# Optimization experiments

Hardware: AMD Instinct MI355X
Metric: run time of the kernel (lower is better)

Reference implementation:

```python
import jax, jax.numpy as jnp
import numpy as np

TEMPLATE_SZ = 7
MAX_SR = 3


def setup_inputs() -> dict:
    key = jax.random.key(0)
    # image-like values in [0, 255) since the module ends with a uint8 cast
    x = jax.random.uniform(key, (2, 1, 192, 192), dtype=jnp.float32) * 255.0
    return {"inputs": x, "search_range": 3}


def reference(inputs, search_range):
    # Equivalent math to: pad(max_sr) -> unfold(k, pad=k//2) -> unfold(s) ->
    # permute -> slice sub-window -> reshape -> uint8.
    # Both zero-pads commute, so fold them into one pad and gather directly,
    # avoiding the huge duplicated double-im2col intermediate.
    k = TEMPLATE_SZ
    max_sr = MAX_SR
    cv = 2 * search_range + 1          # cost_volume_sz
    offset = max_sr - search_range
    B, C, H, W = inputs.shape          # C == 1 (implied by the torch view)
    pad = max_sr + k // 2              # combined zero padding
    Q = jnp.pad(inputs[:, 0].astype(jnp.float32), ((0, 0), (pad, pad), (pad, pad)))
    r = offset + jnp.arange(cv)        # search offsets within max window
    t = jnp.arange(k)                  # template offsets
    # windows[b,i,j,dy,dx,ty,tx] = Q[b, i + r[dy] + ty, j + r[dx] + tx]
    iy = jnp.arange(H)[:, None, None] + r[None, :, None] + t[None, None, :]  # [H, cv, k]
    jx = jnp.arange(W)[:, None, None] + r[None, :, None] + t[None, None, :]  # [W, cv, k]
    win = Q[:, iy[:, None, :, None, :, None], jx[None, :, None, :, None, :]]  # [B,H,W,cv,cv,k,k]
    return win.reshape(B, H, W, cv * cv, k * k).astype(jnp.uint8)
```

## Files before the change

### kernel.cpp

```cpp
#include <hip/hip_runtime.h>


#define KT 7
#define K2 49
#define MAX_SR 3
#define B_ 2
#define H_ 192
#define W_ 192
#define HW (H_ * W_)
#define PAD 6
#define NTHREADS 256
#define RMAX 10
#define PS 17
#define NBLOCKS 768
#define NGROUPS (B_ * H_ * W_ / 4)

typedef int vint4 __attribute__((ext_vector_type(4)));

__global__ __launch_bounds__(NTHREADS) void esw_kernel(
    const float* __restrict__ in, int* __restrict__ out,
    int cv, int offset, int d , int cvmagic )
{
    __shared__ int patch[13 * PS + 4];

    const int tid = threadIdx.x;
    const int bid = blockIdx.x;

    int fe[RMAX][4];
    #pragma unroll
    for (int r = 0; r < RMAX; ++r) {
        int j4 = 4 * (tid + NTHREADS * r);
        #pragma unroll
        for (int u = 0; u < 4; ++u) {
            int jj = j4 + u;
            if (jj >= 4 * d) jj = 4 * d - 1;
            int p_in = (jj >= d) + (jj >= 2 * d) + (jj >= 3 * d);
            int j  = jj - p_in * d;
            int rr = j / K2;
            int tt = j - rr * K2;
            int ry = (rr * cvmagic) >> 16;
            int rx = rr - ry * cv;
            int ty = tt / KT;
            int tx = tt - ty * KT;
            fe[r][u] = (offset + ry + ty) * PS + (offset + rx + tx) + p_in;
        }
    }

    for (int it = 0; it < NGROUPS / NBLOCKS; ++it) {
        const int g = it * NBLOCKS + bid;
        const int pix0 = 4 * g;
        const int b   = pix0 / HW;
        const int rem = pix0 - b * HW;
        const int h   = rem / W_;
        const int w   = rem - h * W_;

        __syncthreads();
        if (tid < 13 * 16) {
            int dy = tid >> 4;
            int dx = tid & 15;
            int y = h + dy - PAD;
            int x = w + dx - PAD;
            int v = 0;
            if ((unsigned)y < (unsigned)H_ && (unsigned)x < (unsigned)W_)
                v = (int)in[b * HW + y * W_ + x];
            patch[dy * PS + dx] = v;
        }
        __syncthreads();

        int* op = out + (long long)g * (long long)(4 * d);
        #pragma unroll
        for (int r = 0; r < RMAX; ++r) {
            int q = tid + NTHREADS * r;
            if (q < d) {
                vint4 v;
                v.x = patch[fe[r][0]];
                v.y = patch[fe[r][1]];
                v.z = patch[fe[r][2]];
                v.w = patch[fe[r][3]];
                *(vint4*)(op + 4 * q) = v;
            }
        }
    }
}

extern "C" void kernel_launch(void* const* d_in, const int* in_sizes, int n_in,
                              void* d_out, int out_size, void* d_ws, size_t ws_size,
                              hipStream_t stream) {
    const float* in = (const float*)d_in[0];
    int* out = (int*)d_out;

    int cv2 = out_size / (B_ * H_ * W_ * K2);
    int cv = 1;
    while (cv * cv < cv2) ++cv;
    int offset = MAX_SR - (cv - 1) / 2;
    int d = cv2 * K2;
    int cvmagic = 65536 / cv + 1;

    esw_kernel<<<NBLOCKS, NTHREADS, 0, stream>>>(in, out, cv, offset, d, cvmagic);
}
```

Before: 702.7 us.

## Precompute gather index table and launch one block per pixel group

Index offsets are computed once by a small separate kernel into workspace, and each esw block loads its offsets as vector loads instead of computing divisions per thread. The persistent loop over 768 blocks is replaced by one 512-thread block per 4-pixel group, which drops the per-iteration syncs and gives a much larger grid. Offsets are prescaled to bytes to save address arithmetic. In exchange it adds a second launch and a table read per block, and relies on workspace being available, falling back to inline computation otherwise.

```diff
diff --git a/kernel.cpp b/kernel.cpp
--- a/kernel.cpp
+++ b/kernel.cpp
@@ -9,76 +9,90 @@
 #define W_ 192
 #define HW (H_ * W_)
 #define PAD 6
-#define NTHREADS 256
-#define RMAX 10
+#define NT 512
+#define RMAX 5
 #define PS 17
-#define NBLOCKS 768
 #define NGROUPS (B_ * H_ * W_ / 4)
+#define TABN (4 * NT * RMAX)
 
 typedef int vint4 __attribute__((ext_vector_type(4)));
 
-__global__ __launch_bounds__(NTHREADS) void esw_kernel(
+__device__ __forceinline__ int tab_entry(int jj, int cv, int offset, int d,
+                                         int cvmagic) {
+    if (jj >= 4 * d) jj = 4 * d - 1;
+    int p_in = (jj >= d) + (jj >= 2 * d) + (jj >= 3 * d);
+    int j  = jj - p_in * d;
+    int rr = j / K2;
+    int tt = j - rr * K2;
+    int ry = (rr * cvmagic) >> 16;
+    int rx = rr - ry * cv;
+    int ty = tt / KT;
+    int tx = tt - ty * KT;
+    return 4 * ((offset + ry + ty) * PS + (offset + rx + tx) + p_in);
+}
+
+__global__ __launch_bounds__(256) void tab_kernel(
+    int* __restrict__ tab, int cv, int offset, int d, int cvmagic)
+{
+    int jj = blockIdx.x * 256 + threadIdx.x;
+    if (jj < TABN) tab[jj] = tab_entry(jj, cv, offset, d, cvmagic);
+}
+
+__global__ __launch_bounds__(NT, 6) void esw_kernel(
     const float* __restrict__ in, int* __restrict__ out,
-    int cv, int offset, int d , int cvmagic )
+    const int* __restrict__ tab,
+    int cv, int offset, int d, int cvmagic)
 {
     __shared__ int patch[13 * PS + 4];
 
     const int tid = threadIdx.x;
-    const int bid = blockIdx.x;
+    const int g   = blockIdx.x;
 
-    int fe[RMAX][4];
-    #pragma unroll
-    for (int r = 0; r < RMAX; ++r) {
-        int j4 = 4 * (tid + NTHREADS * r);
+    vint4 f[RMAX];
+    if (tab) {
         #pragma unroll
-        for (int u = 0; u < 4; ++u) {
-            int jj = j4 + u;
-            if (jj >= 4 * d) jj = 4 * d - 1;
-            int p_in = (jj >= d) + (jj >= 2 * d) + (jj >= 3 * d);
-            int j  = jj - p_in * d;
-            int rr = j / K2;
-            int tt = j - rr * K2;
-            int ry = (rr * cvmagic) >> 16;
-            int rx = rr - ry * cv;
-            int ty = tt / KT;
-            int tx = tt - ty * KT;
-            fe[r][u] = (offset + ry + ty) * PS + (offset + rx + tx) + p_in;
+        for (int r = 0; r < RMAX; ++r)
+            f[r] = *(const vint4*)(tab + 4 * (tid + NT * r));
+    } else {
+        #pragma unroll
+        for (int r = 0; r < RMAX; ++r) {
+            int j4 = 4 * (tid + NT * r);
+            #pragma unroll
+            for (int u = 0; u < 4; ++u)
+                f[r][u] = tab_entry(j4 + u, cv, offset, d, cvmagic);
         }
     }
 
-    for (int it = 0; it < NGROUPS / NBLOCKS; ++it) {
-        const int g = it * NBLOCKS + bid;
-        const int pix0 = 4 * g;
-        const int b   = pix0 / HW;
-        const int rem = pix0 - b * HW;
-        const int h   = rem / W_;
-        const int w   = rem - h * W_;
+    const int pix0 = 4 * g;
+    const int b   = pix0 / HW;
+    const int rem = pix0 - b * HW;
+    const int h   = rem / W_;
+    const int w   = rem - h * W_;
 
-        __syncthreads();
-        if (tid < 13 * 16) {
-            int dy = tid >> 4;
-            int dx = tid & 15;
-            int y = h + dy - PAD;
-            int x = w + dx - PAD;
-            int v = 0;
-            if ((unsigned)y < (unsigned)H_ && (unsigned)x < (unsigned)W_)
-                v = (int)in[b * HW + y * W_ + x];
-            patch[dy * PS + dx] = v;
-        }
-        __syncthreads();
+    if (tid < 13 * 16) {
+        int dy = tid >> 4;
+        int dx = tid & 15;
+        int y = h + dy - PAD;
+        int x = w + dx - PAD;
+        int v = 0;
+        if ((unsigned)y < (unsigned)H_ && (unsigned)x < (unsigned)W_)
+            v = (int)in[b * HW + y * W_ + x];
+        patch[dy * PS + dx] = v;
+    }
+    __syncthreads();
 
-        int* op = out + (long long)g * (long long)(4 * d);
-        #pragma unroll
-        for (int r = 0; r < RMAX; ++r) {
-            int q = tid + NTHREADS * r;
-            if (q < d) {
-                vint4 v;
-                v.x = patch[fe[r][0]];
-                v.y = patch[fe[r][1]];
-                v.z = patch[fe[r][2]];
-                v.w = patch[fe[r][3]];
-                *(vint4*)(op + 4 * q) = v;
-            }
+    int* op = out + (long long)g * (long long)(4 * d);
+    const char* pb = (const char*)patch;
+    #pragma unroll
+    for (int r = 0; r < RMAX; ++r) {
+        int q = tid + NT * r;
+        if (q < d) {
+            vint4 v;
+            v.x = *(const int*)(pb + f[r].x);
+            v.y = *(const int*)(pb + f[r].y);
+            v.z = *(const int*)(pb + f[r].z);
+            v.w = *(const int*)(pb + f[r].w);
+            *(vint4*)(op + 4 * q) = v;
         }
     }
 }
@@ -96,5 +110,9 @@
     int d = cv2 * K2;
     int cvmagic = 65536 / cv + 1;
 
-    esw_kernel<<<NBLOCKS, NTHREADS, 0, stream>>>(in, out, cv, offset, d, cvmagic);
+    int* tab = (ws_size >= (size_t)(TABN * sizeof(int))) ? (int*)d_ws : nullptr;
+    if (tab)
+        tab_kernel<<<(TABN + 255) / 256, 256, 0, stream>>>(tab, cv, offset, d,
+                                                           cvmagic);
+    esw_kernel<<<NGROUPS, NT, 0, stream>>>(in, out, tab, cv, offset, d, cvmagic);
 }
```

New measurement: 696.9 us. No clear change (-0.8%).

## Gather directly from global memory instead of staging patch in LDS

Applied to the files above, without the earlier changes.

Removes the per-group shared-memory patch load and both __syncthreads, so each thread now gathers its 4 values straight from the input through precomputed offsets relative to the image row stride. Interior pixel groups use an unchecked fast path, and border groups clamp coordinates and zero out-of-range values. Block size goes from 256 to 512 threads with 512 blocks and fewer register slots per thread. The cost is more global and L1/L2 gather loads in place of LDS reads, a divergent border path, and 32-bit output indexing.

```diff
diff --git a/kernel.cpp b/kernel.cpp
--- a/kernel.cpp
+++ b/kernel.cpp
@@ -9,75 +9,91 @@
 #define W_ 192
 #define HW (H_ * W_)
 #define PAD 6
-#define NTHREADS 256
-#define RMAX 10
-#define PS 17
-#define NBLOCKS 768
+#define NT 512
+#define NBLOCKS 512
 #define NGROUPS (B_ * H_ * W_ / 4)
+#define NITER (NGROUPS / NBLOCKS)
+#define RMAX 5
 
 typedef int vint4 __attribute__((ext_vector_type(4)));
 
-__global__ __launch_bounds__(NTHREADS) void esw_kernel(
+__device__ __forceinline__ int rel_entry(int jj, int cv, int offset, int d,
+                                         int cvmagic) {
+    if (jj >= 4 * d) jj = 4 * d - 1;
+    int p_in = (jj >= d) + (jj >= 2 * d) + (jj >= 3 * d);
+    int j  = jj - p_in * d;
+    int rr = j / K2;
+    int tt = j - rr * K2;
+    int ry = (rr * cvmagic) >> 16;
+    int rx = rr - ry * cv;
+    int ty = tt / KT;
+    int tx = tt - ty * KT;
+    return (offset + ry + ty) * W_ + (offset + rx + tx) + p_in;
+}
+
+__global__ __launch_bounds__(NT, 2) void esw_kernel(
     const float* __restrict__ in, int* __restrict__ out,
-    int cv, int offset, int d , int cvmagic )
+    int cv, int offset, int d, int cvmagic)
 {
-    __shared__ int patch[13 * PS + 4];
-
     const int tid = threadIdx.x;
     const int bid = blockIdx.x;
 
     int fe[RMAX][4];
     #pragma unroll
-    for (int r = 0; r < RMAX; ++r) {
-        int j4 = 4 * (tid + NTHREADS * r);
+    for (int r = 0; r < RMAX; ++r)
         #pragma unroll
-        for (int u = 0; u < 4; ++u) {
-            int jj = j4 + u;
-            if (jj >= 4 * d) jj = 4 * d - 1;
-            int p_in = (jj >= d) + (jj >= 2 * d) + (jj >= 3 * d);
-            int j  = jj - p_in * d;
-            int rr = j / K2;
-            int tt = j - rr * K2;
-            int ry = (rr * cvmagic) >> 16;
-            int rx = rr - ry * cv;
-            int ty = tt / KT;
-            int tx = tt - ty * KT;
-            fe[r][u] = (offset + ry + ty) * PS + (offset + rx + tx) + p_in;
-        }
-    }
+        for (int u = 0; u < 4; ++u)
+            fe[r][u] = rel_entry(4 * (tid + NT * r) + u, cv, offset, d, cvmagic);
 
-    for (int it = 0; it < NGROUPS / NBLOCKS; ++it) {
+    for (int it = 0; it < NITER; ++it) {
         const int g = it * NBLOCKS + bid;
         const int pix0 = 4 * g;
         const int b   = pix0 / HW;
         const int rem = pix0 - b * HW;
         const int h   = rem / W_;
         const int w   = rem - h * W_;
+        int* op = out + g * (4 * d);
 
-        __syncthreads();
-        if (tid < 13 * 16) {
-            int dy = tid >> 4;
-            int dx = tid & 15;
-            int y = h + dy - PAD;
-            int x = w + dx - PAD;
-            int v = 0;
-            if ((unsigned)y < (unsigned)H_ && (unsigned)x < (unsigned)W_)
-                v = (int)in[b * HW + y * W_ + x];
-            patch[dy * PS + dx] = v;
-        }
-        __syncthreads();
+        const int interior = (h >= PAD) & (h + PAD < H_) &
+                             (w >= PAD) & (w + 9 < W_);
 
-        int* op = out + (long long)g * (long long)(4 * d);
-        #pragma unroll
-        for (int r = 0; r < RMAX; ++r) {
-            int q = tid + NTHREADS * r;
-            if (q < d) {
-                vint4 v;
-                v.x = patch[fe[r][0]];
-                v.y = patch[fe[r][1]];
-                v.z = patch[fe[r][2]];
-                v.w = patch[fe[r][3]];
-                *(vint4*)(op + 4 * q) = v;
+        if (interior) {
+            const float* bp = in + (b * HW + (h - PAD) * W_ + (w - PAD));
+            #pragma unroll
+            for (int r = 0; r < RMAX; ++r) {
+                int q = tid + NT * r;
+                if (q < d) {
+                    vint4 v;
+                    v.x = (int)bp[fe[r][0]];
+                    v.y = (int)bp[fe[r][1]];
+                    v.z = (int)bp[fe[r][2]];
+                    v.w = (int)bp[fe[r][3]];
+                    *(vint4*)(op + 4 * q) = v;
+                }
+            }
+        } else {
+            const int bHW = b * HW;
+            #pragma unroll
+            for (int r = 0; r < RMAX; ++r) {
+                int q = tid + NT * r;
+                if (q < d) {
+                    vint4 v;
+                    #pragma unroll
+                    for (int u = 0; u < 4; ++u) {
+                        int rel = fe[r][u];
+                        int dy  = (int)((((unsigned)rel >> 6) * 0xAAABu) >> 17);
+                        int dx  = rel - dy * W_;
+                        int y   = h - PAD + dy;
+                        int x   = w - PAD + dx;
+                        int inb = ((unsigned)y < (unsigned)H_) &
+                                  ((unsigned)x < (unsigned)W_);
+                        int yc  = y < 0 ? 0 : (y > H_ - 1 ? H_ - 1 : y);
+                        int xc  = x < 0 ? 0 : (x > W_ - 1 ? W_ - 1 : x);
+                        int val = (int)in[bHW + yc * W_ + xc];
+                        v[u] = inb ? val : 0;
+                    }
+                    *(vint4*)(op + 4 * q) = v;
+                }
             }
         }
     }
@@ -96,5 +112,5 @@
     int d = cv2 * K2;
     int cvmagic = 65536 / cv + 1;
 
-    esw_kernel<<<NBLOCKS, NTHREADS, 0, stream>>>(in, out, cv, offset, d, cvmagic);
+    esw_kernel<<<NBLOCKS, NT, 0, stream>>>(in, out, cv, offset, d, cvmagic);
 }
```

Result: slower. 781.8 us (+11.2%).
